# Kernel tuning notes

Hardware: AMD Instinct MI355X
Metric: run time of the kernel (lower is better)

The kernel has to match this reference:

```python
import jax, jax.numpy as jnp
from jax import lax
import numpy as np


def setup_inputs() -> dict:
    key = jax.random.key(0)
    k1, k2 = jax.random.split(key)
    sat_features = jax.random.normal(k1, (128, 4, 64, 16), dtype=jnp.float32)  # [B_s, h, w, c]
    grd_features = jax.random.normal(k2, (128, 4, 64, 16), dtype=jnp.float32)  # [B_g, h, gw, c]
    return {"sat_features": sat_features, "grd_features": grd_features}


def reference(sat_features, grd_features):
    B_s, h, w, c = sat_features.shape
    B_g, gh, gw, gc = grd_features.shape
    assert h == gh and c == gc

    # --- corr: circular cross-correlation over width via conv2d ---
    n = gw - 1
    sat_pad = jnp.concatenate([sat_features, sat_features[:, :, :n, :]], axis=2)  # [B_s,h,w+n,c]
    rhs = jnp.transpose(grd_features, (1, 2, 3, 0))  # HWIO: [h,gw,c,B_g]
    out = lax.conv_general_dilated(
        sat_pad, rhs, window_strides=(1, 1), padding='VALID',
        dimension_numbers=('NHWC', 'HWIO', 'NHWC'))  # [B_s,1,w,B_g]
    corr = out[:, 0, :, :]                  # [B_s, w, B_g]
    orien = jnp.argmax(corr, axis=1)        # [B_s, B_g] int

    # --- crop_sat: circular-shift gather along width, crop to grd width ---
    shift = orien % w                                                   # [B_s,B_g]
    idx = (jnp.arange(gw)[None, None, :] + shift[:, :, None]) % w       # [B_s,B_g,gw]
    # gather: sat_crop[i,j,y,k,ch] = sat_features[i, y, idx[i,j,k], ch]
    sat_crop = jnp.take_along_axis(
        sat_features[:, None],              # [B_s,1,h,w,c]
        idx[:, :, None, :, None],           # [B_s,B_g,1,gw,1]
        axis=3)                             # -> [B_s,B_g,h,gw,c]

    # --- L2 normalize per (sat,grd) pair and squared-chord distance ---
    norm = jnp.sqrt(jnp.sum(sat_crop * sat_crop, axis=(2, 3, 4), keepdims=True))
    sat_matrix = sat_crop / jnp.maximum(norm, 1e-12)
    dot = jnp.sum(sat_matrix * grd_features[None], axis=(2, 3, 4))      # [B_s,B_g]
    distance = 2.0 - 2.0 * dot.T                                        # [B_g,B_s]

    return sat_features, grd_features, distance, orien
```

## Files before the change

### kernel.cpp

```cpp
#include <hip/hip_runtime.h>
#include <math.h>

typedef _Float16 f16;
typedef __attribute__((ext_vector_type(8))) _Float16 f16x8;
typedef __attribute__((ext_vector_type(16))) float f32x16;

#define DIST_OFF  1048576
#define ORI_OFF   1064960
#define SATP_STR  72

#define MFMA(a,b,c) __builtin_amdgcn_mfma_f32_32x32x16_f16((a),(b),(c),0,0,0)

__device__ inline void cvt8(float4 a, float4 b, f16x8* hi, f16x8* lo) {
    float va[8] = {a.x, a.y, a.z, a.w, b.x, b.y, b.z, b.w};
    f16x8 h, l;
    #pragma unroll
    for (int e = 0; e < 8; ++e) {
        f16 hv = (f16)va[e];
        h[e] = hv;
        l[e] = (f16)(va[e] - (float)hv);
    }
    *hi = h; *lo = l;
}

__global__ __launch_bounds__(512, 2) void corr_k(const float* __restrict__ sat,
                                                 const float* __restrict__ grd,
                                                 float* __restrict__ out,
                                                 const float4* __restrict__ satIn,
                                                 const float4* __restrict__ grdIn,
                                                 float4* __restrict__ out4) {
    __shared__ __align__(16) unsigned char smem[131072];
    __shared__ float wred[8];
    __shared__ float rnormS;
    __shared__ float pBest[512];
    __shared__ int   pIdx[512];
    f16* sH = (f16*)smem;
    f16* sL = sH + 127 * SATP_STR;
    float* red = (float*)smem;

    const int tid = threadIdx.x;
    const int s  = blockIdx.x >> 1;
    const int gh = blockIdx.x & 1;
    const int wave = tid >> 6, lane = tid & 63;
    const int m = lane & 31, half = lane >> 5;

    const float* satS = sat + s * 4096;
    float ssq = 0.f;
    #pragma unroll
    for (int r = 0; r < 8; ++r) {
        int idx = r * 512 + tid;
        float v = satS[idx];
        int h = idx >> 10, w = (idx >> 4) & 63, c = idx & 15;
        int col = h * 16 + c;
        f16 hv = (f16)v, lv = (f16)(v - (float)hv);
        sH[w * SATP_STR + col] = hv;
        sL[w * SATP_STR + col] = lv;
        if (w < 63) { sH[(w + 64) * SATP_STR + col] = hv; sL[(w + 64) * SATP_STR + col] = lv; }
        ssq += v * v;
    }
    #pragma unroll
    for (int off = 32; off > 0; off >>= 1) ssq += __shfl_down(ssq, off, 64);
    if (lane == 0) wred[wave] = ssq;
    __syncthreads();
    if (tid == 0) {
        float t = 0.f;
        #pragma unroll
        for (int i = 0; i < 8; ++i) t += wred[i];
        rnormS = 1.f / fmaxf(sqrtf(t), 1e-12f);
    }

    const f16* A0h = sH + m * SATP_STR + half * 8;
    const f16* A0l = sL + m * SATP_STR + half * 8;
    const float* BgA = grd + (gh * 64 + m) * 4096 + half * 8;
    const float* BgB = BgA + 32 * 4096;

    f32x16 z;
    #pragma unroll
    for (int r = 0; r < 16; ++r) z[r] = 0.f;
    f32x16 h00 = z, h01 = z, h10 = z, h11 = z, x00 = z, x01 = z, x10 = z, x11 = z;

    f16x8 ah[2][2], al[2][2], bh[2][2], bl[2][2];

#define LOADA(p, t) { \
    int tc = (t) > 255 ? 255 : (t); \
    int ao = (tc >> 2) * SATP_STR + (tc & 3) * 16; \
    ah[p][0] = *(const f16x8*)(A0h + ao); \
    ah[p][1] = *(const f16x8*)(A0h + ao + 32 * SATP_STR); \
    al[p][0] = *(const f16x8*)(A0l + ao); \
    al[p][1] = *(const f16x8*)(A0l + ao + 32 * SATP_STR); }

#define LOADB(p, t) { \
    int tc = (t) > 255 ? 255 : (t); \
    int fo = (tc & 3) * 1024 + (tc >> 2) * 16; \
    float4 u0 = *(const float4*)(BgA + fo); \
    float4 u1 = *(const float4*)(BgA + fo + 4); \
    float4 w0 = *(const float4*)(BgB + fo); \
    float4 w1 = *(const float4*)(BgB + fo + 4); \
    cvt8(u0, u1, &bh[p][0], &bl[p][0]); \
    cvt8(w0, w1, &bh[p][1], &bl[p][1]); }

#define STEP(p) { \
    h00 = MFMA(ah[p][0], bh[p][0], h00); \
    h01 = MFMA(ah[p][0], bh[p][1], h01); \
    h10 = MFMA(ah[p][1], bh[p][0], h10); \
    h11 = MFMA(ah[p][1], bh[p][1], h11); \
    x00 = MFMA(ah[p][0], bl[p][0], x00); x00 = MFMA(al[p][0], bh[p][0], x00); \
    x01 = MFMA(ah[p][0], bl[p][1], x01); x01 = MFMA(al[p][0], bh[p][1], x01); \
    x10 = MFMA(ah[p][1], bl[p][0], x10); x10 = MFMA(al[p][1], bh[p][0], x10); \
    x11 = MFMA(ah[p][1], bl[p][1], x11); x11 = MFMA(al[p][1], bh[p][1], x11); }

    const int t0 = wave * 32;
    LOADA(0, t0) LOADB(0, t0)
    #pragma unroll 4
    for (int t = t0; t < t0 + 32; t += 2) {
        LOADA(1, t + 1) LOADB(1, t + 1)
        STEP(0)
        LOADA(0, t + 2) LOADB(0, t + 2)
        STEP(1)
    }
    h00 = h00 + x00; h01 = h01 + x01; h10 = h10 + x10; h11 = h11 + x11;

    __syncthreads();
    float* rw = red + wave * 4096;
    #pragma unroll
    for (int r = 0; r < 16; ++r) {
        int j0 = (r & 3) + 8 * (r >> 2) + 4 * half;
        rw[j0 * 64 + m]             = h00[r];
        rw[j0 * 64 + 32 + m]        = h01[r];
        rw[(j0 + 32) * 64 + m]      = h10[r];
        rw[(j0 + 32) * 64 + 32 + m] = h11[r];
    }
    __syncthreads();
    #pragma unroll
    for (int i = 0; i < 8; ++i) {
        int c = i * 512 + tid;
        float v = red[c]         + red[c + 4096]  + red[c + 8192]  + red[c + 12288]
                + red[c + 16384] + red[c + 20480] + red[c + 24576] + red[c + 28672];
        red[c] = v;
    }
    __syncthreads();

    {
        int g = tid & 63, jq = tid >> 6;
        int jb = jq * 8;
        float best = red[jb * 64 + g];
        int bj = jb;
        #pragma unroll
        for (int jj = 1; jj < 8; ++jj) {
            float v = red[(jb + jj) * 64 + g];
            if (v > best) { best = v; bj = jb + jj; }
        }
        pBest[tid] = best; pIdx[tid] = bj;
    }
    __syncthreads();
    if (tid < 64) {
        int g = tid;
        float best = pBest[g]; int bj = pIdx[g];
        #pragma unroll
        for (int jq = 1; jq < 8; ++jq) {
            float v = pBest[jq * 64 + g];
            if (v > best) { best = v; bj = pIdx[jq * 64 + g]; }
        }
        float dot = best * rnormS;
        int gg = gh * 64 + g;
        out[DIST_OFF + gg * 128 + s] = 2.f - 2.f * dot;
        out[ORI_OFF + s * 128 + gg]  = (float)bj;
    }

    {
        int i = blockIdx.x * 512 + tid;
        out4[i] = satIn[i];
        out4[131072 + i] = grdIn[i];
    }
}

extern "C" void kernel_launch(void* const* d_in, const int* in_sizes, int n_in,
                              void* d_out, int out_size, void* d_ws, size_t ws_size,
                              hipStream_t stream) {
    const float* sat = (const float*)d_in[0];
    const float* grd = (const float*)d_in[1];
    float* out = (float*)d_out;
    corr_k<<<256, 512, 0, stream>>>(sat, grd, out,
                                    (const float4*)sat, (const float4*)grd, (float4*)out);
}
```

Measured before the change: 92.04 us.

## Split grd batch into quarters per block and shrink shared-memory reduction

Doubles the grid so each block handles one sat sample against 32 grd samples. Each wave now computes a single 32x32 MFMA tile over a quarter of K instead of a 2x2 tile set, and only four-way K partials go through a much smaller shared buffer. Less LDS per block allows higher occupancy (launch bounds raised to 4 blocks) and removes the 8-way 128KB reduction. In exchange the sat tile is staged and the fp16 split conversion is done by twice as many blocks, the grd fp32-to-fp16 conversion is now redone for each 32-row sat tile, and a single-lane 64-step argmax replaces the two-level parallel argmax.

Measured after the change: 119.3 us. +29.6%, slower.

```diff
diff --git a/kernel.cpp b/kernel.cpp
--- a/kernel.cpp
+++ b/kernel.cpp
@@ -23,26 +23,26 @@
     *hi = h; *lo = l;
 }
 
-__global__ __launch_bounds__(512, 2) void corr_k(const float* __restrict__ sat,
+__global__ __launch_bounds__(512, 4) void corr_k(const float* __restrict__ sat,
                                                  const float* __restrict__ grd,
                                                  float* __restrict__ out,
                                                  const float4* __restrict__ satIn,
                                                  const float4* __restrict__ grdIn,
                                                  float4* __restrict__ out4) {
-    __shared__ __align__(16) unsigned char smem[131072];
+    __shared__ __align__(16) unsigned char smem[36864];
     __shared__ float wred[8];
     __shared__ float rnormS;
-    __shared__ float pBest[512];
-    __shared__ int   pIdx[512];
     f16* sH = (f16*)smem;
     f16* sL = sH + 127 * SATP_STR;
-    float* red = (float*)smem;
+    float* pPart = (float*)smem;
+    float* corrF = (float*)smem + 6144;
 
     const int tid = threadIdx.x;
-    const int s  = blockIdx.x >> 1;
-    const int gh = blockIdx.x & 1;
+    const int s  = blockIdx.x >> 2;
+    const int gq = blockIdx.x & 3;
     const int wave = tid >> 6, lane = tid & 63;
     const int m = lane & 31, half = lane >> 5;
+    const int jt = wave & 1, kq = wave >> 1;
 
     const float* satS = sat + s * 4096;
     float ssq = 0.f;
@@ -69,108 +69,78 @@
         rnormS = 1.f / fmaxf(sqrtf(t), 1e-12f);
     }
 
-    const f16* A0h = sH + m * SATP_STR + half * 8;
-    const f16* A0l = sL + m * SATP_STR + half * 8;
-    const float* BgA = grd + (gh * 64 + m) * 4096 + half * 8;
-    const float* BgB = BgA + 32 * 4096;
+    const f16* A0h = sH + (jt * 32 + m) * SATP_STR + half * 8;
+    const f16* A0l = sL + (jt * 32 + m) * SATP_STR + half * 8;
+    const float* Bg = grd + (gq * 32 + m) * 4096 + half * 8;
 
-    f32x16 z;
+    f32x16 hA, xA;
     #pragma unroll
-    for (int r = 0; r < 16; ++r) z[r] = 0.f;
-    f32x16 h00 = z, h01 = z, h10 = z, h11 = z, x00 = z, x01 = z, x10 = z, x11 = z;
+    for (int r = 0; r < 16; ++r) { hA[r] = 0.f; xA[r] = 0.f; }
 
-    f16x8 ah[2][2], al[2][2], bh[2][2], bl[2][2];
+    f16x8 ah[2], al[2], bh, bl;
+    float4 br[2][2];
 
-#define LOADA(p, t) { \
-    int tc = (t) > 255 ? 255 : (t); \
-    int ao = (tc >> 2) * SATP_STR + (tc & 3) * 16; \
-    ah[p][0] = *(const f16x8*)(A0h + ao); \
-    ah[p][1] = *(const f16x8*)(A0h + ao + 32 * SATP_STR); \
-    al[p][0] = *(const f16x8*)(A0l + ao); \
-    al[p][1] = *(const f16x8*)(A0l + ao + 32 * SATP_STR); }
+#define LOADA(p, t) { int ao = ((t) >> 2) * SATP_STR + ((t) & 3) * 16; \
+    ah[p] = *(const f16x8*)(A0h + ao); al[p] = *(const f16x8*)(A0l + ao); }
+#define LOADB(p, t) { int fo = ((t) & 3) * 1024 + ((t) >> 2) * 16; \
+    br[p][0] = *(const float4*)(Bg + fo); br[p][1] = *(const float4*)(Bg + fo + 4); }
 
-#define LOADB(p, t) { \
-    int tc = (t) > 255 ? 255 : (t); \
-    int fo = (tc & 3) * 1024 + (tc >> 2) * 16; \
-    float4 u0 = *(const float4*)(BgA + fo); \
-    float4 u1 = *(const float4*)(BgA + fo + 4); \
-    float4 w0 = *(const float4*)(BgB + fo); \
-    float4 w1 = *(const float4*)(BgB + fo + 4); \
-    cvt8(u0, u1, &bh[p][0], &bl[p][0]); \
-    cvt8(w0, w1, &bh[p][1], &bl[p][1]); }
-
-#define STEP(p) { \
-    h00 = MFMA(ah[p][0], bh[p][0], h00); \
-    h01 = MFMA(ah[p][0], bh[p][1], h01); \
-    h10 = MFMA(ah[p][1], bh[p][0], h10); \
-    h11 = MFMA(ah[p][1], bh[p][1], h11); \
-    x00 = MFMA(ah[p][0], bl[p][0], x00); x00 = MFMA(al[p][0], bh[p][0], x00); \
-    x01 = MFMA(ah[p][0], bl[p][1], x01); x01 = MFMA(al[p][0], bh[p][1], x01); \
-    x10 = MFMA(ah[p][1], bl[p][0], x10); x10 = MFMA(al[p][1], bh[p][0], x10); \
-    x11 = MFMA(ah[p][1], bl[p][1], x11); x11 = MFMA(al[p][1], bh[p][1], x11); }
-
-    const int t0 = wave * 32;
-    LOADA(0, t0) LOADB(0, t0)
+    const int tb = kq * 64, tmax = tb + 63;
+    LOADA(0, tb) LOADB(0, tb)
     #pragma unroll 4
-    for (int t = t0; t < t0 + 32; t += 2) {
-        LOADA(1, t + 1) LOADB(1, t + 1)
-        STEP(0)
-        LOADA(0, t + 2) LOADB(0, t + 2)
-        STEP(1)
+    for (int tt = 0; tt < 64; ++tt) {
+        int tn = (tt < 63) ? tb + tt + 1 : tmax;
+        LOADA((tt + 1) & 1, tn)
+        LOADB((tt + 1) & 1, tn)
+        cvt8(br[tt & 1][0], br[tt & 1][1], &bh, &bl);
+        hA = MFMA(ah[tt & 1], bh, hA);
+        xA = MFMA(ah[tt & 1], bl, xA);
+        xA = MFMA(al[tt & 1], bh, xA);
     }
-    h00 = h00 + x00; h01 = h01 + x01; h10 = h10 + x10; h11 = h11 + x11;
+    f32x16 p = hA + xA;
 
     __syncthreads();
-    float* rw = red + wave * 4096;
-    #pragma unroll
-    for (int r = 0; r < 16; ++r) {
-        int j0 = (r & 3) + 8 * (r >> 2) + 4 * half;
-        rw[j0 * 64 + m]             = h00[r];
-        rw[j0 * 64 + 32 + m]        = h01[r];
-        rw[(j0 + 32) * 64 + m]      = h10[r];
-        rw[(j0 + 32) * 64 + 32 + m] = h11[r];
+
+    if (kq != 0) {
+        float* dst = pPart + (jt * 3 + (kq - 1)) * 1024;
+        #pragma unroll
+        for (int r = 0; r < 16; ++r) {
+            int j0 = (r & 3) + 8 * (r >> 2) + 4 * half;
+            dst[j0 * 32 + m] = p[r];
+        }
     }
     __syncthreads();
-    #pragma unroll
-    for (int i = 0; i < 8; ++i) {
-        int c = i * 512 + tid;
-        float v = red[c]         + red[c + 4096]  + red[c + 8192]  + red[c + 12288]
-                + red[c + 16384] + red[c + 20480] + red[c + 24576] + red[c + 28672];
-        red[c] = v;
+    if (kq == 0) {
+        const float* q1 = pPart + (jt * 3 + 0) * 1024;
+        const float* q2 = pPart + (jt * 3 + 1) * 1024;
+        const float* q3 = pPart + (jt * 3 + 2) * 1024;
+        #pragma unroll
+        for (int r = 0; r < 16; ++r) {
+            int j0 = (r & 3) + 8 * (r >> 2) + 4 * half;
+            int a = j0 * 32 + m;
+            float v = ((p[r] + q1[a]) + q2[a]) + q3[a];
+            corrF[(jt * 32 + j0) * 32 + m] = v;
+        }
     }
     __syncthreads();
 
-    {
-        int g = tid & 63, jq = tid >> 6;
-        int jb = jq * 8;
-        float best = red[jb * 64 + g];
-        int bj = jb;
-        #pragma unroll
-        for (int jj = 1; jj < 8; ++jj) {
-            float v = red[(jb + jj) * 64 + g];
-            if (v > best) { best = v; bj = jb + jj; }
-        }
-        pBest[tid] = best; pIdx[tid] = bj;
-    }
-    __syncthreads();
-    if (tid < 64) {
+    if (tid < 32) {
         int g = tid;
-        float best = pBest[g]; int bj = pIdx[g];
-        #pragma unroll
-        for (int jq = 1; jq < 8; ++jq) {
-            float v = pBest[jq * 64 + g];
-            if (v > best) { best = v; bj = pIdx[jq * 64 + g]; }
+        float best = corrF[g];
+        int bj = 0;
+        for (int j = 1; j < 64; ++j) {
+            float v = corrF[j * 32 + g];
+            if (v > best) { best = v; bj = j; }
         }
         float dot = best * rnormS;
-        int gg = gh * 64 + g;
+        int gg = gq * 32 + g;
         out[DIST_OFF + gg * 128 + s] = 2.f - 2.f * dot;
         out[ORI_OFF + s * 128 + gg]  = (float)bj;
     }
 
     {
         int i = blockIdx.x * 512 + tid;
-        out4[i] = satIn[i];
-        out4[131072 + i] = grdIn[i];
+        out4[i] = (i < 131072) ? satIn[i] : grdIn[i - 131072];
     }
 }
 
@@ -180,6 +150,6 @@
     const float* sat = (const float*)d_in[0];
     const float* grd = (const float*)d_in[1];
     float* out = (float*)d_out;
-    corr_k<<<256, 512, 0, stream>>>(sat, grd, out,
+    corr_k<<<512, 512, 0, stream>>>(sat, grd, out,
                                     (const float4*)sat, (const float4*)grd, (float4*)out);
 }
```
